# Performance work log

Hardware: AMD Instinct MI355X
Metric: run time of the kernel (lower is better)

## Reference

```python
import jax, jax.numpy as jnp
from jax import lax
import numpy as np

N, H, K, B, L = 8192, 256, 100, 32, 128
FS = [1, 2, 3, 4]
W2 = 2 * H + 10  # conv kernel width; padded input width (2H+10) == kernel width -> out width 1


def setup_inputs() -> dict:
    key = jax.random.key(0)
    ks = jax.random.split(key, 16)
    inp = {}
    # scale adj by 1/sqrt(N) so layer1 activations stay O(1) (keeps softmax numerically sane)
    inp["adj"] = jax.random.normal(ks[0], (N, N), jnp.float32) / np.float32(np.sqrt(N))
    # xavier-uniform-scale init for the node embedding parameter
    inp["embedding"] = jax.random.normal(ks[1], (N, H), jnp.float32) * np.float32(np.sqrt(2.0 / (N + H)))
    inp["q_idx"] = jax.random.randint(ks[2], (B, L), 0, N, dtype=jnp.int32)
    inp["a_idx"] = jax.random.randint(ks[3], (B, L), 0, N, dtype=jnp.int32)
    for i, fs in enumerate(FS):
        fan_in = fs * W2
        inp[f"conv_w{i}"] = jax.random.normal(ks[4 + i], (K, 1, fs, W2), jnp.float32) / np.float32(np.sqrt(fan_in))
        inp[f"conv_b{i}"] = jnp.zeros((K,), jnp.float32)
    inp["dense_w"] = jax.random.normal(ks[12], (4 * K * 2, 2), jnp.float32) * np.float32(0.02)
    inp["dense_b"] = jnp.zeros((2,), jnp.float32)
    return inp


def _cnn_branch(t, conv_ws, conv_bs):
    # t: [B, 1, L, 2H]; each conv has padding=5 on both spatial dims,
    # kernel width == 2H+10 so output width == 1; relu then max-pool over full height.
    outs = []
    for w, b in zip(conv_ws, conv_bs):
        y = lax.conv_general_dilated(t, w, (1, 1), [(5, 5), (5, 5)],
                                     dimension_numbers=("NCHW", "OIHW", "NCHW"))
        y = jax.nn.relu(y + b[None, :, None, None])  # [B, K, L+10-fs+1, 1]
        outs.append(jnp.max(y, axis=(2, 3)))  # [B, K]
    return jnp.concatenate(outs, axis=1)  # [B, 4K]


def reference(adj, embedding, q_idx, a_idx,
              conv_w0, conv_b0, conv_w1, conv_b1,
              conv_w2, conv_b2, conv_w3, conv_b3,
              dense_w, dense_b):
    conv_ws = [conv_w0, conv_w1, conv_w2, conv_w3]
    conv_bs = [conv_b0, conv_b1, conv_b2, conv_b3]
    # featureless GCN layer: layer1 = A @ E  -> [N, H]
    layer1 = adj @ embedding
    # per-sample word gathers (ragged in original, fixed length L here)
    Q = layer1[q_idx]  # [B, L, H]
    A = layer1[a_idx]  # [B, L, H]
    # soft alignment: score = Q A^T; wq = softmax rows; wa = softmax(score.T, dim=1) == softmax over axis 1
    score = jnp.einsum("blh,bmh->blm", Q, A)
    wq = jax.nn.softmax(score, axis=2)
    wa = jax.nn.softmax(score, axis=1)
    EQ = jnp.einsum("blm,bmh->blh", wq, A)  # aligned encoding of Q
    EA = jnp.einsum("blm,blh->bmh", wa, Q)  # aligned encoding of A
    # match features: squared diff ++ elementwise product -> [B, 1, L, 2H]
    tq = jnp.concatenate([(Q - EQ) ** 2, Q * EQ], axis=-1)[:, None]
    ta = jnp.concatenate([(A - EA) ** 2, A * EA], axis=-1)[:, None]
    # dropout is identity in eval mode
    q_re = jax.nn.relu(_cnn_branch(tq, conv_ws, conv_bs))  # [B, 4K]
    a_re = jax.nn.relu(_cnn_branch(ta, conv_ws, conv_bs))  # [B, 4K]
    re = jnp.concatenate([q_re, a_re], axis=1)  # [B, 8K]
    logits = re @ dense_w + dense_b  # [B, 2]  (F.relu(score) in original is a discarded no-op)
    return jax.nn.log_softmax(logits, axis=1)
```

## Files before the change

kernel.cpp:

```cpp
#include <hip/hip_runtime.h>
#include <hip/hip_bf16.h>
#include <stdint.h>

typedef unsigned short u16;
typedef __attribute__((ext_vector_type(8))) short bf16x8;
typedef __attribute__((ext_vector_type(4))) float f32x4;

#define NN 8192
#define HH 256
#define KK 100
#define BB 32
#define LL 128
#define NPAD 1024
#define SPLITK 8
#define KCH (NN / SPLITK)
#define STEPS1 (KCH / 64)
#define STEPS2 (512 / 64)

__device__ __forceinline__ u16 f2bf_rne(float x) {
  union { __hip_bfloat16 h; u16 u; } v;
  v.h = __float2bfloat16(x);
  return v.u;
}

__device__ __forceinline__ float bf2f(u16 u) {
  union { unsigned int i; float f; } v;
  v.i = ((unsigned int)u) << 16;
  return v.f;
}

__device__ __forceinline__ bf16x8 pack8(f32x4 a, f32x4 b) {
  bf16x8 r;
  r[0] = (short)f2bf_rne(a.x); r[1] = (short)f2bf_rne(a.y);
  r[2] = (short)f2bf_rne(a.z); r[3] = (short)f2bf_rne(a.w);
  r[4] = (short)f2bf_rne(b.x); r[5] = (short)f2bf_rne(b.y);
  r[6] = (short)f2bf_rne(b.z); r[7] = (short)f2bf_rne(b.w);
  return r;
}

__device__ __forceinline__ void gld16(const void* g, void* l) {
  __builtin_amdgcn_global_load_lds(
      (const __attribute__((address_space(1))) unsigned int*)g,
      (__attribute__((address_space(3))) unsigned int*)l, 16, 0, 0);
}

__global__ __launch_bounds__(256) void convert_embT(const float* __restrict__ emb,
                                                    u16* __restrict__ embT) {
  __shared__ float t[64][65];
  const int tid = threadIdx.x;
  const int k0 = blockIdx.x * 64, n0 = blockIdx.y * 64;
#pragma unroll
  for (int i = 0; i < 16; ++i) {
    int idx = i * 256 + tid;
    int r = idx >> 6, c = idx & 63;
    t[r][c] = emb[(size_t)(k0 + r) * HH + n0 + c];
  }
  __syncthreads();
#pragma unroll
  for (int i = 0; i < 16; ++i) {
    int idx = i * 256 + tid;
    int r = idx >> 6, c = idx & 63;
    embT[(size_t)(n0 + r) * NN + k0 + c] = f2bf_rne(t[c][r]);
  }
}

__global__ __launch_bounds__(1024) void dedup_rows(const int* __restrict__ q_idx,
                                                   const int* __restrict__ a_idx,
                                                   int* __restrict__ rank,
                                                   int* __restrict__ rows,
                                                   int* __restrict__ muniq) {
  __shared__ unsigned bm[256];
  __shared__ int cnt[1024];
  __shared__ int total;
  const int tid = threadIdx.x;
  if (tid < 256) bm[tid] = 0u;
  __syncthreads();
  for (int i = tid; i < BB * LL; i += 1024) {
    int q = q_idx[i];
    atomicOr(&bm[q >> 5], 1u << (q & 31));
  }
  for (int i = tid; i < BB * LL; i += 1024) {
    int a = a_idx[i];
    atomicOr(&bm[a >> 5], 1u << (a & 31));
  }
  __syncthreads();
  const unsigned w = bm[tid >> 2];
  const unsigned byte = (w >> ((tid & 3) * 8)) & 0xffu;
  const int myc = __popc(byte);
  cnt[tid] = myc;
  __syncthreads();
  for (int off = 1; off < 1024; off <<= 1) {
    int v = (tid >= off) ? cnt[tid - off] : 0;
    __syncthreads();
    cnt[tid] += v;
    __syncthreads();
  }
  if (tid == 1023) total = cnt[1023];
  int base = cnt[tid] - myc;
#pragma unroll
  for (int j = 0; j < 8; ++j) {
    int n = tid * 8 + j;
    int bit = (byte >> j) & 1;
    rank[n] = base;
    if (bit) rows[base++] = n;
  }
  __syncthreads();
  if (tid == 0) *muniq = total;
  if (tid < 64) rows[total + tid] = 0;
}

__global__ __launch_bounds__(512, 6) void gemm_layer1c(const float* __restrict__ adj,
                                                       const u16* __restrict__ embT,
                                                       const int* __restrict__ rows,
                                                       const int* __restrict__ muniq,
                                                       float* __restrict__ parts) {
  __shared__ __align__(16) float As[64 * 64];
  __shared__ __align__(16) u16 Bs[256 * 64];
  const int tid = threadIdx.x;
  const int lane = tid & 63, wid = tid >> 6;
  const int wm = wid >> 2, wn = wid & 3;
  const int wg = blockIdx.x;
  const int sk = wg & 7;
  const int mt = wg >> 3;
  const int m0 = mt * 64;
  const int M = *muniq;
  if (m0 >= M) return;
  const int kbeg = sk * KCH;

  f32x4 acc[2][4];
  const f32x4 zf = {0.f, 0.f, 0.f, 0.f};
#pragma unroll
  for (int i = 0; i < 2; ++i)
#pragma unroll
    for (int j = 0; j < 4; ++j) acc[i][j] = zf;

  int aRowLoc[2], aGsrc[2];
  const float* aSrc[2];
#pragma unroll
  for (int j = 0; j < 2; ++j) {
    int t = wid * 2 + j;
    aRowLoc[j] = t * 4 + (lane >> 4);
    aGsrc[j] = (lane & 15) ^ (aRowLoc[j] & 15);
    int grow = rows[m0 + aRowLoc[j]];
    aSrc[j] = adj + (size_t)grow * NN + kbeg + aGsrc[j] * 4;
  }
  const u16* bSrc[4];
#pragma unroll
  for (int j = 0; j < 4; ++j) {
    int t = wid * 4 + j;
    int rowB = t * 8 + (lane >> 3);
    int g = (lane & 7) ^ (rowB & 7);
    bSrc[j] = embT + (size_t)rowB * NN + kbeg + g * 8;
  }

  for (int s = 0; s < STEPS1; ++s) {
    const int ks = s * 64;
#pragma unroll
    for (int j = 0; j < 2; ++j)
      gld16(aSrc[j] + ks, (void*)&As[(wid * 2 + j) * 256]);
#pragma unroll
    for (int j = 0; j < 4; ++j)
      gld16(bSrc[j] + ks, (void*)&Bs[(wid * 4 + j) * 512]);
    __syncthreads();
#pragma unroll
    for (int kk = 0; kk < 64; kk += 32) {
      bf16x8 af[2], bfr[4];
      const int g0 = (kk >> 2) + ((lane >> 4) << 1);
#pragma unroll
      for (int mi = 0; mi < 2; ++mi) {
        int row = wm * 32 + mi * 16 + (lane & 15);
        f32x4 p0 = *reinterpret_cast<const f32x4*>(&As[row * 64 + ((g0 ^ (row & 15)) << 2)]);
        f32x4 p1 = *reinterpret_cast<const f32x4*>(&As[row * 64 + (((g0 + 1) ^ (row & 15)) << 2)]);
        af[mi] = pack8(p0, p1);
      }
      const int gb = (kk >> 3) + (lane >> 4);
#pragma unroll
      for (int ni = 0; ni < 4; ++ni) {
        int row = wn * 64 + ni * 16 + (lane & 15);
        bfr[ni] = *reinterpret_cast<const bf16x8*>(&Bs[row * 64 + ((gb ^ (row & 7)) << 3)]);
      }
#pragma unroll
      for (int mi = 0; mi < 2; ++mi)
#pragma unroll
        for (int ni = 0; ni < 4; ++ni)
          acc[mi][ni] = __builtin_amdgcn_mfma_f32_16x16x32_bf16(af[mi], bfr[ni], acc[mi][ni], 0, 0, 0);
    }
    __syncthreads();
  }

  float* outp = parts + (size_t)sk * ((size_t)NN * HH);
  const int r0 = (lane >> 4) << 2;
  const int coln = wn * 64 + (lane & 15);
#pragma unroll
  for (int mi = 0; mi < 2; ++mi)
#pragma unroll
    for (int ni = 0; ni < 4; ++ni)
#pragma unroll
      for (int r = 0; r < 4; ++r)
        outp[(size_t)(m0 + wm * 32 + mi * 16 + r0 + r) * HH + coln + ni * 16] = acc[mi][ni][r];
}

__global__ __launch_bounds__(256) void gather_qa(const float* __restrict__ parts,
                                                 const int* __restrict__ q_idx,
                                                 const int* __restrict__ a_idx,
                                                 const int* __restrict__ rank,
                                                 u16* __restrict__ Qbf, u16* __restrict__ Abf) {
  const int rb = blockIdx.x;
  const bool isA = rb >= BB * LL;
  const int r = isA ? rb - BB * LL : rb;
  const int idx = (isA ? a_idx : q_idx)[r];
  const int cidx = rank[idx];
  const int tid = threadIdx.x;
  float s = 0.f;
#pragma unroll
  for (int p = 0; p < SPLITK; ++p)
    s += parts[(size_t)p * ((size_t)NN * HH) + (size_t)cidx * HH + tid];
  (isA ? Abf : Qbf)[(size_t)r * HH + tid] = f2bf_rne(s);
}

__global__ __launch_bounds__(512) void attn_fused(const u16* __restrict__ Qbf,
                                                  const u16* __restrict__ Abf,
                                                  u16* __restrict__ wqbf,
                                                  u16* __restrict__ watbf) {
  __shared__ __align__(16) char lraw[131072];
  u16* Qs = (u16*)lraw;
  u16* As = (u16*)(lraw + 65536);
  float* sc = (float*)lraw;
  const int b = blockIdx.x;
  const int tid = threadIdx.x;
  const int lane = tid & 63, wid = tid >> 6;
  const int wm = wid >> 2, wn = wid & 3;

  const u16* qsrc = Qbf + (size_t)b * (LL * HH);
  const u16* asrc = Abf + (size_t)b * (LL * HH);
#pragma unroll
  for (int i = 0; i < 8; ++i) {
    int gf = i * 512 + tid;
    int l = gf >> 5, g = gf & 31;
    int gp = g ^ (l & 7);
    *reinterpret_cast<bf16x8*>(&Qs[l * 256 + gp * 8]) = *reinterpret_cast<const bf16x8*>(qsrc + l * 256 + g * 8);
    *reinterpret_cast<bf16x8*>(&As[l * 256 + gp * 8]) = *reinterpret_cast<const bf16x8*>(asrc + l * 256 + g * 8);
  }
  __syncthreads();

  f32x4 acc[4][2];
  const f32x4 zf = {0.f, 0.f, 0.f, 0.f};
#pragma unroll
  for (int i = 0; i < 4; ++i)
#pragma unroll
    for (int j = 0; j < 2; ++j) acc[i][j] = zf;

#pragma unroll
  for (int ks = 0; ks < 8; ++ks) {
    bf16x8 af[4], bfr[2];
#pragma unroll
    for (int mi = 0; mi < 4; ++mi) {
      int row = wm * 64 + mi * 16 + (lane & 15);
      int g = ks * 4 + (lane >> 4);
      af[mi] = *reinterpret_cast<const bf16x8*>(&Qs[row * 256 + (g ^ (row & 7)) * 8]);
    }
#pragma unroll
    for (int ni = 0; ni < 2; ++ni) {
      int row = wn * 32 + ni * 16 + (lane & 15);
      int g = ks * 4 + (lane >> 4);
      bfr[ni] = *reinterpret_cast<const bf16x8*>(&As[row * 256 + (g ^ (row & 7)) * 8]);
    }
#pragma unroll
    for (int mi = 0; mi < 4; ++mi)
#pragma unroll
      for (int ni = 0; ni < 2; ++ni)
        acc[mi][ni] = __builtin_amdgcn_mfma_f32_16x16x32_bf16(af[mi], bfr[ni], acc[mi][ni], 0, 0, 0);
  }
  __syncthreads();

  const int r0 = (lane >> 4) << 2;
#pragma unroll
  for (int mi = 0; mi < 4; ++mi)
#pragma unroll
    for (int ni = 0; ni < 2; ++ni) {
      int m = wn * 32 + ni * 16 + (lane & 15);
#pragma unroll
      for (int r = 0; r < 4; ++r) {
        int l = wm * 64 + mi * 16 + r0 + r;
        sc[l * 132 + m] = acc[mi][ni][r];
      }
    }
  __syncthreads();

  {
    const int l = tid >> 2, j = tid & 3;
    const int base = l * 132 + j * 32;
    float mx = -3.4e38f;
#pragma unroll 8
    for (int c = 0; c < 32; ++c) mx = fmaxf(mx, sc[base + c]);
    mx = fmaxf(mx, __shfl_xor(mx, 1));
    mx = fmaxf(mx, __shfl_xor(mx, 2));
    float sum = 0.f;
#pragma unroll 8
    for (int c = 0; c < 32; ++c) sum += expf(sc[base + c] - mx);
    sum += __shfl_xor(sum, 1);
    sum += __shfl_xor(sum, 2);
    float inv = 1.f / sum;
    u16* o = wqbf + (size_t)b * (LL * LL) + l * 128 + j * 32;
#pragma unroll 8
    for (int c = 0; c < 32; ++c) o[c] = f2bf_rne(expf(sc[base + c] - mx) * inv);
  }
  {
    const int m = tid >> 2, j = tid & 3;
    float mx = -3.4e38f;
#pragma unroll 8
    for (int r = 0; r < 32; ++r) mx = fmaxf(mx, sc[(j * 32 + r) * 132 + m]);
    mx = fmaxf(mx, __shfl_xor(mx, 1));
    mx = fmaxf(mx, __shfl_xor(mx, 2));
    float sum = 0.f;
#pragma unroll 8
    for (int r = 0; r < 32; ++r) sum += expf(sc[(j * 32 + r) * 132 + m] - mx);
    sum += __shfl_xor(sum, 1);
    sum += __shfl_xor(sum, 2);
    float inv = 1.f / sum;
    u16* o = watbf + (size_t)b * (LL * LL) + m * 128 + j * 32;
#pragma unroll 8
    for (int r = 0; r < 32; ++r) o[r] = f2bf_rne(expf(sc[(j * 32 + r) * 132 + m] - mx) * inv);
  }
}

__global__ __launch_bounds__(512) void align_mfma(const u16* __restrict__ wqbf,
                                                  const u16* __restrict__ watbf,
                                                  const u16* __restrict__ Qbf,
                                                  const u16* __restrict__ Abf,
                                                  u16* __restrict__ Tbf) {
  __shared__ __align__(16) u16 wsh[128 * 128];
  __shared__ __align__(16) u16 srcT[256 * 140];
  const int bid = blockIdx.x;
  const int side = bid >> 5, b = bid & 31;
  const int tid = threadIdx.x;
  const int lane = tid & 63, wid = tid >> 6;
  const int wm = wid >> 2, wn = wid & 3;

  const u16* wsrc = (side ? watbf : wqbf) + (size_t)b * (LL * LL);
  const u16* ssrc = (side ? Qbf : Abf) + (size_t)b * (LL * HH);
  const u16* msrc = (side ? Abf : Qbf) + (size_t)b * (LL * HH);

#pragma unroll
  for (int i = 0; i < 4; ++i) {
    int gf = i * 512 + tid;
    int row = gf >> 4, g = gf & 15;
    int gp = g ^ (row & 7);
    *reinterpret_cast<bf16x8*>(&wsh[row * 128 + gp * 8]) = *reinterpret_cast<const bf16x8*>(wsrc + row * 128 + g * 8);
  }
#pragma unroll
  for (int i = 0; i < 8; ++i) {
    int gf = i * 512 + tid;
    int j = gf >> 5, g = gf & 31;
    bf16x8 v = *reinterpret_cast<const bf16x8*>(ssrc + j * 256 + g * 8);
#pragma unroll
    for (int e = 0; e < 8; ++e) srcT[(g * 8 + e) * 140 + j] = (u16)v[e];
  }
  __syncthreads();

  f32x4 acc[4][4];
  const f32x4 zf = {0.f, 0.f, 0.f, 0.f};
#pragma unroll
  for (int i = 0; i < 4; ++i)
#pragma unroll
    for (int j = 0; j < 4; ++j) acc[i][j] = zf;

#pragma unroll
  for (int ks = 0; ks < 4; ++ks) {
    bf16x8 af[4], bfr[4];
#pragma unroll
    for (int mi = 0; mi < 4; ++mi) {
      int row = wm * 64 + mi * 16 + (lane & 15);
      int g = ks * 4 + (lane >> 4);
      af[mi] = *reinterpret_cast<const bf16x8*>(&wsh[row * 128 + (g ^ (row & 7)) * 8]);
    }
#pragma unroll
    for (int ni = 0; ni < 4; ++ni) {
      int h = wn * 64 + ni * 16 + (lane & 15);
      int k = ks * 32 + ((lane >> 4) << 3);
      bfr[ni] = *reinterpret_cast<const bf16x8*>(&srcT[h * 140 + k]);
    }
#pragma unroll
    for (int mi = 0; mi < 4; ++mi)
#pragma unroll
      for (int ni = 0; ni < 4; ++ni)
        acc[mi][ni] = __builtin_amdgcn_mfma_f32_16x16x32_bf16(af[mi], bfr[ni], acc[mi][ni], 0, 0, 0);
  }

  u16* outp = Tbf + (size_t)(side * 4096 + b * 128) * 512;
  const int r0 = (lane >> 4) << 2;
#pragma unroll
  for (int mi = 0; mi < 4; ++mi)
#pragma unroll
    for (int ni = 0; ni < 4; ++ni) {
      int h = wn * 64 + ni * 16 + (lane & 15);
#pragma unroll
      for (int r = 0; r < 4; ++r) {
        int i2 = wm * 64 + mi * 16 + r0 + r;
        float mv = bf2f(msrc[(size_t)i2 * HH + h]);
        float e = acc[mi][ni][r];
        float d = mv - e;
        outp[(size_t)i2 * 512 + h] = f2bf_rne(d * d);
        outp[(size_t)i2 * 512 + 256 + h] = f2bf_rne(mv * e);
      }
    }
}

__global__ __launch_bounds__(256) void prep_wcat(const float* __restrict__ w0,
                                                 const float* __restrict__ w1,
                                                 const float* __restrict__ w2,
                                                 const float* __restrict__ w3,
                                                 u16* __restrict__ Wcat) {
  const int kr = blockIdx.x;
  const int tid = threadIdx.x;
  u16* out = Wcat + (size_t)kr * 512;
  if (kr >= KK * 10) {
    out[tid] = 0;
    out[tid + 256] = 0;
    return;
  }
  const int k = kr / 10, s = kr % 10;
  const float* w;
  int r, fs;
  if (s < 1)      { w = w0; r = s;     fs = 1; }
  else if (s < 3) { w = w1; r = s - 1; fs = 2; }
  else if (s < 6) { w = w2; r = s - 3; fs = 3; }
  else            { w = w3; r = s - 6; fs = 4; }
  const float* src = w + ((size_t)k * fs + r) * 522 + 5;
  out[tid] = f2bf_rne(src[tid]);
  out[tid + 256] = f2bf_rne(src[tid + 256]);
}

__global__ __launch_bounds__(512, 4) void gemm_conv(const u16* __restrict__ Tbf,
                                                    const u16* __restrict__ Wcat,
                                                    float* __restrict__ D) {
  __shared__ __align__(16) u16 As[128 * 64];
  __shared__ __align__(16) u16 Bs[256 * 64];
  const int tid = threadIdx.x;
  const int lane = tid & 63, wid = tid >> 6;
  const int wm = wid >> 2, wn = wid & 3;
  const int m0 = blockIdx.x * 128;
  const int n0 = blockIdx.y * 256;

  f32x4 acc[4][4];
  const f32x4 zf = {0.f, 0.f, 0.f, 0.f};
#pragma unroll
  for (int i = 0; i < 4; ++i)
#pragma unroll
    for (int j = 0; j < 4; ++j) acc[i][j] = zf;

  const int browL = (lane >> 3);
  const int bkL = (lane & 7) << 3;

  for (int s = 0; s < STEPS2; ++s) {
    const int ks = s * 64;
#pragma unroll
    for (int j = 0; j < 2; ++j) {
      int rowA = (wid << 4) + (j << 3) + browL;
      int kA = bkL ^ ((rowA & 7) << 3);
      gld16(Tbf + (size_t)(m0 + rowA) * 512 + ks + kA, (void*)&As[(wid * 2 + j) * 512]);
    }
#pragma unroll
    for (int j = 0; j < 4; ++j) {
      int rowB = (wid << 5) + (j << 3) + browL;
      int kB = bkL ^ ((rowB & 7) << 3);
      gld16(Wcat + (size_t)(n0 + rowB) * 512 + ks + kB, (void*)&Bs[(wid * 4 + j) * 512]);
    }
    __syncthreads();
#pragma unroll
    for (int kk = 0; kk < 64; kk += 32) {
      const int krow = kk + ((lane >> 4) << 3);
      bf16x8 af[4], bfr[4];
#pragma unroll
      for (int mi = 0; mi < 4; ++mi) {
        int row = wm * 64 + mi * 16 + (lane & 15);
        af[mi] = *reinterpret_cast<const bf16x8*>(&As[row * 64 + (krow ^ ((row & 7) << 3))]);
      }
#pragma unroll
      for (int ni = 0; ni < 4; ++ni) {
        int row = wn * 64 + ni * 16 + (lane & 15);
        bfr[ni] = *reinterpret_cast<const bf16x8*>(&Bs[row * 64 + (krow ^ ((row & 7) << 3))]);
      }
#pragma unroll
      for (int mi = 0; mi < 4; ++mi)
#pragma unroll
        for (int ni = 0; ni < 4; ++ni)
          acc[mi][ni] = __builtin_amdgcn_mfma_f32_16x16x32_bf16(af[mi], bfr[ni], acc[mi][ni], 0, 0, 0);
    }
    __syncthreads();
  }

  const int r0 = (lane >> 4) << 2;
  const int coln = n0 + wn * 64 + (lane & 15);
#pragma unroll
  for (int mi = 0; mi < 4; ++mi)
#pragma unroll
    for (int ni = 0; ni < 4; ++ni)
#pragma unroll
      for (int r = 0; r < 4; ++r)
        D[(size_t)(m0 + wm * 64 + mi * 16 + r0 + r) * NPAD + coln + ni * 16] = acc[mi][ni][r];
}

__global__ __launch_bounds__(256) void reduce_conv(const float* __restrict__ D,
                                                   const float* __restrict__ b0,
                                                   const float* __restrict__ b1,
                                                   const float* __restrict__ b2,
                                                   const float* __restrict__ b3,
                                                   float* __restrict__ re) {
  __shared__ float tile[128][101];
  const int pair = blockIdx.y;
  const int sel = pair >> 5, b = pair & 31;
  const int kc = blockIdx.x;
  const int tid = threadIdx.x;
  const int rowbase = sel * (BB * LL) + b * LL;
  const int c0 = kc * 100;
  for (int idx = tid; idx < 12800; idx += 256) {
    int r = idx / 100, c = idx - r * 100;
    tile[r][c] = D[(size_t)(rowbase + r) * NPAD + c0 + c];
  }
  __syncthreads();
  const int wid = tid >> 6, lane = tid & 63;
  const int offt[4] = {0, 1, 3, 6};
  const int fst[4] = {1, 2, 3, 4};
  for (int o = wid; o < 40; o += 4) {
    const int kk = o >> 2, f = o & 3;
    const int fs = fst[f], off = offt[f];
    const int kg = kc * 10 + kk;
    const float bias = (f == 0 ? b0 : f == 1 ? b1 : f == 2 ? b2 : b3)[kg];
    const int col = kk * 10 + off;
    const int outh = 139 - fs;
    float best = 0.f;
    for (int i = lane; i < outh; i += 64) {
      float s = bias;
#pragma unroll 4
      for (int r = 0; r < 4; ++r) {
        if (r < fs) {
          int j = i + r - 5;
          if (j >= 0 && j < LL) s += tile[j][col + r];
        }
      }
      best = fmaxf(best, s);
    }
    best = fmaxf(best, 0.f);
#pragma unroll
    for (int d = 32; d; d >>= 1) best = fmaxf(best, __shfl_xor(best, d));
    if (lane == 0) re[(size_t)b * 800 + sel * 400 + f * 100 + kg] = best;
  }
}

__global__ __launch_bounds__(64) void dense_logsm(const float* __restrict__ re,
                                                  const float* __restrict__ dw,
                                                  const float* __restrict__ db,
                                                  float* __restrict__ out) {
  const int b = blockIdx.x;
  const int lane = threadIdx.x;
  const float* r = re + (size_t)b * 800;
  float a0 = 0.f, a1 = 0.f;
  for (int j = lane; j < 800; j += 64) {
    float rv = r[j];
    a0 += rv * dw[j * 2];
    a1 += rv * dw[j * 2 + 1];
  }
#pragma unroll
  for (int d = 32; d; d >>= 1) {
    a0 += __shfl_xor(a0, d);
    a1 += __shfl_xor(a1, d);
  }
  if (lane == 0) {
    a0 += db[0];
    a1 += db[1];
    float mx = fmaxf(a0, a1);
    float lse = mx + logf(expf(a0 - mx) + expf(a1 - mx));
    out[b * 2] = a0 - lse;
    out[b * 2 + 1] = a1 - lse;
  }
}

static const size_t OFF_PARTS = 0;
static const size_t OFF_D     = 0;
static const size_t OFF_QBF   = 67108864;
static const size_t OFF_ABF   = OFF_QBF + 2097152;
static const size_t OFF_WQB   = OFF_ABF + 2097152;
static const size_t OFF_WAB   = OFF_WQB + 1048576;
static const size_t OFF_RE    = OFF_WAB + 1048576;
static const size_t OFF_TBF   = OFF_RE + 102400;
static const size_t OFF_WCAT  = OFF_TBF + 8388608;
static const size_t OFF_EMBT  = OFF_WCAT + 1048576;
static const size_t OFF_RANK  = OFF_EMBT + 4194304;
static const size_t OFF_ROWS  = OFF_RANK + 32768;
static const size_t OFF_MUNIQ = OFF_ROWS + 33024;

extern "C" void kernel_launch(void* const* d_in, const int* in_sizes, int n_in,
                              void* d_out, int out_size, void* d_ws, size_t ws_size,
                              hipStream_t stream) {
  (void)in_sizes; (void)n_in; (void)out_size; (void)ws_size;
  const float* adj  = (const float*)d_in[0];
  const float* emb  = (const float*)d_in[1];
  const int* q_idx  = (const int*)d_in[2];
  const int* a_idx  = (const int*)d_in[3];
  const float* cw0 = (const float*)d_in[4];
  const float* cb0 = (const float*)d_in[5];
  const float* cw1 = (const float*)d_in[6];
  const float* cb1 = (const float*)d_in[7];
  const float* cw2 = (const float*)d_in[8];
  const float* cb2 = (const float*)d_in[9];
  const float* cw3 = (const float*)d_in[10];
  const float* cb3 = (const float*)d_in[11];
  const float* dw = (const float*)d_in[12];
  const float* db = (const float*)d_in[13];
  float* out = (float*)d_out;

  char* ws = (char*)d_ws;
  float* parts = (float*)(ws + OFF_PARTS);
  float* Dbuf  = (float*)(ws + OFF_D);
  u16* Qbf     = (u16*)(ws + OFF_QBF);
  u16* Abf     = (u16*)(ws + OFF_ABF);
  u16* wqbf    = (u16*)(ws + OFF_WQB);
  u16* watbf   = (u16*)(ws + OFF_WAB);
  float* re    = (float*)(ws + OFF_RE);
  u16* Tbf     = (u16*)(ws + OFF_TBF);
  u16* Wcat    = (u16*)(ws + OFF_WCAT);
  u16* embT    = (u16*)(ws + OFF_EMBT);
  int* rank    = (int*)(ws + OFF_RANK);
  int* rows    = (int*)(ws + OFF_ROWS);
  int* muniq   = (int*)(ws + OFF_MUNIQ);

  convert_embT<<<dim3(128, 4), 256, 0, stream>>>(emb, embT);
  dedup_rows<<<1, 1024, 0, stream>>>(q_idx, a_idx, rank, rows, muniq);
  prep_wcat<<<1024, 256, 0, stream>>>(cw0, cw1, cw2, cw3, Wcat);
  gemm_layer1c<<<128 * SPLITK, 512, 0, stream>>>(adj, embT, rows, muniq, parts);
  gather_qa<<<2 * BB * LL, 256, 0, stream>>>(parts, q_idx, a_idx, rank, Qbf, Abf);
  attn_fused<<<BB, 512, 0, stream>>>(Qbf, Abf, wqbf, watbf);
  align_mfma<<<64, 512, 0, stream>>>(wqbf, watbf, Qbf, Abf, Tbf);
  gemm_conv<<<dim3(64, 4), 512, 0, stream>>>(Tbf, Wcat, Dbuf);
  reduce_conv<<<dim3(10, 64), 256, 0, stream>>>(Dbuf, cb0, cb1, cb2, cb3, re);
  dense_logsm<<<BB, 64, 0, stream>>>(re, dw, db, out);
}
```

Before: 157.9 us.

## Restructure layer1 GEMM: 128-row tiles, A fragments loaded directly from global

The layer1 GEMM now uses 128-row M tiles, with each wave owning 16 rows across all 256 output columns. The adj operand is read straight from global memory into registers and converted to bf16 there, so the A tile no longer passes through LDS. Only the embedding tile is staged in LDS, in 128-wide K chunks. This halves the number of workgroups and cuts how often each embedding chunk is reloaded, at the cost of more accumulator registers and lower occupancy. Direct global loads of A inside the MFMA loop may expose memory latency.

```diff
diff --git a/kernel.cpp b/kernel.cpp
--- a/kernel.cpp
+++ b/kernel.cpp
@@ -14,7 +14,6 @@
 #define NPAD 1024
 #define SPLITK 8
 #define KCH (NN / SPLITK)
-#define STEPS1 (KCH / 64)
 #define STEPS2 (512 / 64)
 
 __device__ __forceinline__ u16 f2bf_rne(float x) {
@@ -106,98 +105,67 @@
   }
   __syncthreads();
   if (tid == 0) *muniq = total;
-  if (tid < 64) rows[total + tid] = 0;
-}
-
-__global__ __launch_bounds__(512, 6) void gemm_layer1c(const float* __restrict__ adj,
+  if (tid < 128) rows[total + tid] = 0;
+}
+
+__global__ __launch_bounds__(512, 4) void gemm_layer1d(const float* __restrict__ adj,
                                                        const u16* __restrict__ embT,
                                                        const int* __restrict__ rows,
                                                        const int* __restrict__ muniq,
                                                        float* __restrict__ parts) {
-  __shared__ __align__(16) float As[64 * 64];
-  __shared__ __align__(16) u16 Bs[256 * 64];
+  __shared__ __align__(16) u16 Bs[256 * 128];
   const int tid = threadIdx.x;
   const int lane = tid & 63, wid = tid >> 6;
-  const int wm = wid >> 2, wn = wid & 3;
   const int wg = blockIdx.x;
   const int sk = wg & 7;
   const int mt = wg >> 3;
-  const int m0 = mt * 64;
+  const int m0 = mt * 128;
   const int M = *muniq;
   if (m0 >= M) return;
   const int kbeg = sk * KCH;
 
-  f32x4 acc[2][4];
-  const f32x4 zf = {0.f, 0.f, 0.f, 0.f};
-#pragma unroll
-  for (int i = 0; i < 2; ++i)
-#pragma unroll
-    for (int j = 0; j < 4; ++j) acc[i][j] = zf;
-
-  int aRowLoc[2], aGsrc[2];
-  const float* aSrc[2];
-#pragma unroll
-  for (int j = 0; j < 2; ++j) {
-    int t = wid * 2 + j;
-    aRowLoc[j] = t * 4 + (lane >> 4);
-    aGsrc[j] = (lane & 15) ^ (aRowLoc[j] & 15);
-    int grow = rows[m0 + aRowLoc[j]];
-    aSrc[j] = adj + (size_t)grow * NN + kbeg + aGsrc[j] * 4;
-  }
-  const u16* bSrc[4];
-#pragma unroll
-  for (int j = 0; j < 4; ++j) {
-    int t = wid * 4 + j;
-    int rowB = t * 8 + (lane >> 3);
-    int g = (lane & 7) ^ (rowB & 7);
-    bSrc[j] = embT + (size_t)rowB * NN + kbeg + g * 8;
-  }
-
-  for (int s = 0; s < STEPS1; ++s) {
-    const int ks = s * 64;
-#pragma unroll
-    for (int j = 0; j < 2; ++j)
-      gld16(aSrc[j] + ks, (void*)&As[(wid * 2 + j) * 256]);
-#pragma unroll
-    for (int j = 0; j < 4; ++j)
-      gld16(bSrc[j] + ks, (void*)&Bs[(wid * 4 + j) * 512]);
+  const int myrow = rows[m0 + wid * 16 + (lane & 15)];
+  const float* aBase = adj + (size_t)myrow * NN + kbeg + ((lane >> 4) << 3);
+
+  f32x4 acc[16];
+#pragma unroll
+  for (int i = 0; i < 16; ++i) acc[i] = (f32x4){0.f, 0.f, 0.f, 0.f};
+
+  for (int kb = 0; kb < 8; ++kb) {
+#pragma unroll
+    for (int j = 0; j < 8; ++j) {
+      int t = wid * 8 + j;
+      int row = t * 4 + (lane >> 4);
+      int g = (lane & 15) ^ (row & 15);
+      gld16(embT + (size_t)row * NN + kbeg + kb * 128 + g * 8, (void*)&Bs[t * 512]);
+    }
     __syncthreads();
 #pragma unroll
-    for (int kk = 0; kk < 64; kk += 32) {
-      bf16x8 af[2], bfr[4];
-      const int g0 = (kk >> 2) + ((lane >> 4) << 1);
-#pragma unroll
-      for (int mi = 0; mi < 2; ++mi) {
-        int row = wm * 32 + mi * 16 + (lane & 15);
-        f32x4 p0 = *reinterpret_cast<const f32x4*>(&As[row * 64 + ((g0 ^ (row & 15)) << 2)]);
-        f32x4 p1 = *reinterpret_cast<const f32x4*>(&As[row * 64 + (((g0 + 1) ^ (row & 15)) << 2)]);
-        af[mi] = pack8(p0, p1);
+    for (int kk = 0; kk < 4; ++kk) {
+      const f32x4* ap = reinterpret_cast<const f32x4*>(aBase + kb * 128 + kk * 32);
+      f32x4 a0 = ap[0], a1 = ap[1];
+      bf16x8 af = pack8(a0, a1);
+#pragma unroll
+      for (int ni = 0; ni < 16; ++ni) {
+        int row = ni * 16 + (lane & 15);
+        int slot = (kk * 4 + (lane >> 4)) ^ (row & 15);
+        bf16x8 bfr = *reinterpret_cast<const bf16x8*>(&Bs[row * 128 + slot * 8]);
+        acc[ni] = __builtin_amdgcn_mfma_f32_16x16x32_bf16(af, bfr, acc[ni], 0, 0, 0);
       }
-      const int gb = (kk >> 3) + (lane >> 4);
-#pragma unroll
-      for (int ni = 0; ni < 4; ++ni) {
-        int row = wn * 64 + ni * 16 + (lane & 15);
-        bfr[ni] = *reinterpret_cast<const bf16x8*>(&Bs[row * 64 + ((gb ^ (row & 7)) << 3)]);
-      }
-#pragma unroll
-      for (int mi = 0; mi < 2; ++mi)
-#pragma unroll
-        for (int ni = 0; ni < 4; ++ni)
-          acc[mi][ni] = __builtin_amdgcn_mfma_f32_16x16x32_bf16(af[mi], bfr[ni], acc[mi][ni], 0, 0, 0);
     }
     __syncthreads();
   }
 
   float* outp = parts + (size_t)sk * ((size_t)NN * HH);
   const int r0 = (lane >> 4) << 2;
-  const int coln = wn * 64 + (lane & 15);
-#pragma unroll
-  for (int mi = 0; mi < 2; ++mi)
-#pragma unroll
-    for (int ni = 0; ni < 4; ++ni)
-#pragma unroll
-      for (int r = 0; r < 4; ++r)
-        outp[(size_t)(m0 + wm * 32 + mi * 16 + r0 + r) * HH + coln + ni * 16] = acc[mi][ni][r];
+  const int mrow = m0 + wid * 16 + r0;
+#pragma unroll
+  for (int ni = 0; ni < 16; ++ni) {
+    int col = ni * 16 + (lane & 15);
+#pragma unroll
+    for (int r = 0; r < 4; ++r)
+      outp[(size_t)(mrow + r) * HH + col] = acc[ni][r];
+  }
 }
 
 __global__ __launch_bounds__(256) void gather_qa(const float* __restrict__ parts,
@@ -588,7 +556,7 @@
 static const size_t OFF_EMBT  = OFF_WCAT + 1048576;
 static const size_t OFF_RANK  = OFF_EMBT + 4194304;
 static const size_t OFF_ROWS  = OFF_RANK + 32768;
-static const size_t OFF_MUNIQ = OFF_ROWS + 33024;
+static const size_t OFF_MUNIQ = OFF_ROWS + 33280;
 
 extern "C" void kernel_launch(void* const* d_in, const int* in_sizes, int n_in,
                               void* d_out, int out_size, void* d_ws, size_t ws_size,
@@ -628,7 +596,7 @@
   convert_embT<<<dim3(128, 4), 256, 0, stream>>>(emb, embT);
   dedup_rows<<<1, 1024, 0, stream>>>(q_idx, a_idx, rank, rows, muniq);
   prep_wcat<<<1024, 256, 0, stream>>>(cw0, cw1, cw2, cw3, Wcat);
-  gemm_layer1c<<<128 * SPLITK, 512, 0, stream>>>(adj, embT, rows, muniq, parts);
+  gemm_layer1d<<<64 * SPLITK, 512, 0, stream>>>(adj, embT, rows, muniq, parts);
   gather_qa<<<2 * BB * LL, 256, 0, stream>>>(parts, q_idx, a_idx, rank, Qbf, Abf);
   attn_fused<<<BB, 512, 0, stream>>>(Qbf, Abf, wqbf, watbf);
   align_mfma<<<64, 512, 0, stream>>>(wqbf, watbf, Qbf, Abf, Tbf);
```

Result: slower. 166.7 us (+5.6%).
